# Performance work log

Measured on AMD Instinct MI355X. Metric: run time of the kernel, lower is better.

## Reference

```python
import jax, jax.numpy as jnp
import numpy as np

MAX_LOGIT = 30.0
COV_WEIGHT = 1.0


def setup_inputs() -> dict:
    key = jax.random.key(0)
    ks = jax.random.split(key, 8)
    B, T, S, H = 8, 100, 400, 256
    sc = 1.0 / np.sqrt(H)
    return {
        "decoder_outputs": jax.random.normal(ks[0], (B, T, H), jnp.float32),
        "encoder_outputs": jax.random.normal(ks[1], (B, S, H), jnp.float32),
        "src_mask": jnp.zeros((B, S), dtype=bool),
        "W_h": jax.random.normal(ks[2], (H, H), jnp.float32) * sc,
        "W_s": jax.random.normal(ks[3], (H, H), jnp.float32) * sc,
        "w_c": jax.random.normal(ks[4], (H,), jnp.float32) * sc,  # Linear(1,H) weight
        "v": jax.random.normal(ks[5], (H,), jnp.float32) * sc,    # Linear(H,1) weight
        "b_attn": jnp.zeros((H,), jnp.float32),
    }


def reference(decoder_outputs, encoder_outputs, src_mask, W_h, W_s, w_c, v, b_attn):
    B, T, H = decoder_outputs.shape
    S = encoder_outputs.shape[1]
    neg_inf = jnp.float32(-jnp.inf)

    Wh = jnp.einsum('bsh,hk->bsk', encoder_outputs, W_h)   # [B,S,H]
    Ws = jnp.einsum('bth,hk->btk', decoder_outputs, W_s)   # [B,T,H]
    # E_base: [B,T,S,H]
    E_base = Wh[:, None, :, :] + Ws[:, :, None, :] + b_attn

    def logits(x):
        e = jnp.einsum('btsh,h->bts', jnp.tanh(x), v)
        e = jnp.clip(e, -MAX_LOGIT, MAX_LOGIT)
        return jnp.where(src_mask[:, None, :], neg_inf, e)

    A_prelim = jax.nn.softmax(logits(E_base), axis=-1)      # [B,T,S]
    cum = jnp.cumsum(A_prelim, axis=1)
    cov_shifted = jnp.concatenate(
        [jnp.zeros((B, 1, S), A_prelim.dtype), cum[:, :-1, :]], axis=1)  # [B,T,S]

    # W_c applied to scalar coverage: outer product with w_c -> [B,T,S,H]
    E_final = logits(E_base + cov_shifted[..., None] * w_c)
    A_final = jax.nn.softmax(E_final, axis=-1)              # [B,T,S]

    context = jnp.einsum('bts,bsh->bth', A_final, encoder_outputs)
    cov_loss = (COV_WEIGHT * jnp.sum(jnp.minimum(A_final, cov_shifted), axis=-1).mean())[None]
    return context, A_final, cov_loss
```

## Files before the change

kernel.cpp:

```cpp
#include <hip/hip_runtime.h>
#include <math.h>

#define B_ 8
#define T_ 100
#define S_ 400
#define H_ 256
#define BT_ (B_ * T_)
#define MAXL 30.0f
#define K_EXP 2.885390081777927f

#define AF_OFF (BT_ * H_)
#define LOSS_OFF (BT_ * H_ + BT_ * S_)

#define WHT_OFF 0
#define WSB_OFF (B_ * H_ * S_)
#define ACOV_OFF (WSB_OFF + BT_ * H_)

__device__ __forceinline__ float wave_sum(float p) {
#pragma unroll
    for (int off = 32; off; off >>= 1) p += __shfl_xor(p, off, 64);
    return p;
}

__device__ __forceinline__ float wave_max(float p) {
#pragma unroll
    for (int off = 32; off; off >>= 1) p = fmaxf(p, __shfl_xor(p, off, 64));
    return p;
}

#define ROWS 4
__global__ __launch_bounds__(256) void k_gemm(
    const float* __restrict__ dec, const float* __restrict__ enc,
    const float* __restrict__ W_h, const float* __restrict__ W_s,
    const float* __restrict__ b_attn,
    float* __restrict__ WhT, float* __restrict__ Wsb) {
    const int tid = threadIdx.x;
    const int blk = blockIdx.x;
    const int NB_ENC = (B_ * S_) / ROWS;

    float a0 = 0.f, a1 = 0.f, a2 = 0.f, a3 = 0.f;

    if (blk < NB_ENC) {
        const int r0 = blk * ROWS;
        const int b = r0 / S_, s0 = r0 - b * S_;
        const float* in = enc + (size_t)r0 * H_;
        const float* Wp = W_h + tid;
#pragma unroll 8
        for (int h = 0; h < H_; ++h) {
            float w = Wp[(size_t)h * H_];
            a0 = fmaf(in[h], w, a0);
            a1 = fmaf(in[H_ + h], w, a1);
            a2 = fmaf(in[2 * H_ + h], w, a2);
            a3 = fmaf(in[3 * H_ + h], w, a3);
        }
        float* o = WhT + ((size_t)b * H_ + tid) * S_ + s0;
        o[0] = K_EXP * a0;
        o[1] = K_EXP * a1;
        o[2] = K_EXP * a2;
        o[3] = K_EXP * a3;
    } else {
        const int bt0 = (blk - NB_ENC) * ROWS;
        const float* in = dec + (size_t)bt0 * H_;
        const float* Wp = W_s + tid;
        const float bias = b_attn[tid];
#pragma unroll 8
        for (int h = 0; h < H_; ++h) {
            float w = Wp[(size_t)h * H_];
            a0 = fmaf(in[h], w, a0);
            a1 = fmaf(in[H_ + h], w, a1);
            a2 = fmaf(in[2 * H_ + h], w, a2);
            a3 = fmaf(in[3 * H_ + h], w, a3);
        }
        Wsb[(size_t)(bt0 + 0) * H_ + tid] = K_EXP * (a0 + bias);
        Wsb[(size_t)(bt0 + 1) * H_ + tid] = K_EXP * (a1 + bias);
        Wsb[(size_t)(bt0 + 2) * H_ + tid] = K_EXP * (a2 + bias);
        Wsb[(size_t)(bt0 + 3) * H_ + tid] = K_EXP * (a3 + bias);
    }
}

__global__ __launch_bounds__(512) void k_prelim(
    const float* __restrict__ WhT, const float* __restrict__ Wsb,
    const float* __restrict__ v,
    const unsigned char* __restrict__ mask,
    float* __restrict__ A) {
    __shared__ float red[16];
    const int blk = blockIdx.x;
    const int b = blk & 7;
    const int t = blk >> 3;
    const int bt = b * T_ + t;
    const int tid = threadIdx.x;
    const int lane = tid & 63;
    const int wid = tid >> 6;
    const int s = tid;
    const bool act = (s < S_);

    const float4 vv4 = *reinterpret_cast<const float4*>(v + 4 * lane);
    const float sumv = wave_sum((vv4.x + vv4.y) + (vv4.z + vv4.w));

    const float* Wsr = Wsb + (size_t)bt * H_;
    float acc = 0.f;
    if (act) {
        const float* wcol = WhT + (size_t)b * H_ * S_ + s;
#pragma unroll 8
        for (int h = 0; h < H_; ++h) {
            float w = wcol[(size_t)h * S_];
            float r = __builtin_amdgcn_rcpf(__builtin_amdgcn_exp2f(w + Wsr[h]) + 1.0f);
            acc = fmaf(r, v[h], acc);
        }
    }

    float e = -INFINITY;
    if (act) {
        e = fminf(fmaxf(sumv - 2.f * acc, -MAXL), MAXL);
        if (mask[(size_t)b * S_ + s]) e = -INFINITY;
    }

    float mx = wave_max(e);
    if (lane == 0) red[wid] = mx;
    __syncthreads();
    mx = fmaxf(fmaxf(fmaxf(red[0], red[1]), fmaxf(red[2], red[3])),
               fmaxf(fmaxf(red[4], red[5]), fmaxf(red[6], red[7])));

    float p = act ? __expf(e - mx) : 0.f;
    float sum = wave_sum(p);
    if (lane == 0) red[8 + wid] = sum;
    __syncthreads();
    sum = ((red[8] + red[9]) + (red[10] + red[11])) +
          ((red[12] + red[13]) + (red[14] + red[15]));
    const float inv = __builtin_amdgcn_rcpf(sum);

    if (act) A[(size_t)bt * S_ + s] = p * inv;
}

__global__ __launch_bounds__(64) void k_cumsum(float* __restrict__ A,
                                               float* __restrict__ out) {
    const int idx = blockIdx.x * 64 + threadIdx.x;
    if (idx == 0) out[LOSS_OFF] = 0.f;
    if (idx >= B_ * S_) return;
    const int b = idx / S_;
    const int s = idx - b * S_;
    float* col = A + (size_t)b * T_ * S_ + s;
    float run = 0.f;
#pragma unroll 10
    for (int t = 0; t < T_; ++t) {
        float a = col[(size_t)t * S_];
        col[(size_t)t * S_] = run;
        run += a;
    }
}

__global__ __launch_bounds__(512) void k_final(
    const float* __restrict__ WhT, const float* __restrict__ Wsb,
    const float* __restrict__ v, const float* __restrict__ w_c,
    const float* __restrict__ cov,
    const unsigned char* __restrict__ mask,
    const float* __restrict__ enc,
    float* __restrict__ out) {
    __shared__ float e_lds[S_];
    __shared__ float ctx_part[H_];
    __shared__ float red[16];
    const int blk = blockIdx.x;
    const int b = blk & 7;
    const int t = blk >> 3;
    const int bt = b * T_ + t;
    const int tid = threadIdx.x;
    const int lane = tid & 63;
    const int wid = tid >> 6;
    const int s = tid;
    const bool act = (s < S_);

    const float4 vv4 = *reinterpret_cast<const float4*>(v + 4 * lane);
    const float sumv = wave_sum((vv4.x + vv4.y) + (vv4.z + vv4.w));

    float c = 0.f;
    if (act) c = cov[(size_t)bt * S_ + s];
    const float ck = K_EXP * c;

    const float* Wsr = Wsb + (size_t)bt * H_;
    float acc = 0.f;
    if (act) {
        const float* wcol = WhT + (size_t)b * H_ * S_ + s;
#pragma unroll 8
        for (int h = 0; h < H_; ++h) {
            float w = wcol[(size_t)h * S_];
            float arg = fmaf(ck, w_c[h], w + Wsr[h]);
            float r = __builtin_amdgcn_rcpf(__builtin_amdgcn_exp2f(arg) + 1.0f);
            acc = fmaf(r, v[h], acc);
        }
    }

    float e = -INFINITY;
    if (act) {
        e = fminf(fmaxf(sumv - 2.f * acc, -MAXL), MAXL);
        if (mask[(size_t)b * S_ + s]) e = -INFINITY;
    }

    float mx = wave_max(e);
    if (lane == 0) red[wid] = mx;
    __syncthreads();
    mx = fmaxf(fmaxf(fmaxf(red[0], red[1]), fmaxf(red[2], red[3])),
               fmaxf(fmaxf(red[4], red[5]), fmaxf(red[6], red[7])));

    float p = act ? __expf(e - mx) : 0.f;
    float sum = wave_sum(p);
    if (lane == 0) red[8 + wid] = sum;
    __syncthreads();
    sum = ((red[8] + red[9]) + (red[10] + red[11])) +
          ((red[12] + red[13]) + (red[14] + red[15]));
    const float inv = __builtin_amdgcn_rcpf(sum);

    const float a = act ? p * inv : 0.f;

    float lp = act ? fminf(a, c) : 0.f;
    lp = wave_sum(lp);
    if (lane == 0) red[wid] = lp;

    if (act) {
        e_lds[s] = a;
        out[AF_OFF + (size_t)bt * S_ + s] = a;
    }
    __syncthreads();

    if (tid == 0) {
        float tot = ((red[0] + red[1]) + (red[2] + red[3])) +
                    ((red[4] + red[5]) + (red[6] + red[7]));
        atomicAdd(out + LOSS_OFF, tot * (1.0f / (B_ * T_)));
    }

    const int h = tid & (H_ - 1);
    const int half = tid >> 8;
    const int s0 = half * (S_ / 2);
    const float* eb = enc + ((size_t)b * S_ + s0) * H_ + h;
    float ca = 0.f, cb = 0.f, cc = 0.f, cd = 0.f;
#pragma unroll 5
    for (int j = 0; j < S_ / 2; j += 4) {
        ca = fmaf(e_lds[s0 + j], eb[(size_t)j * H_], ca);
        cb = fmaf(e_lds[s0 + j + 1], eb[(size_t)(j + 1) * H_], cb);
        cc = fmaf(e_lds[s0 + j + 2], eb[(size_t)(j + 2) * H_], cc);
        cd = fmaf(e_lds[s0 + j + 3], eb[(size_t)(j + 3) * H_], cd);
    }
    if (half == 0) ctx_part[h] = (ca + cb) + (cc + cd);
    __syncthreads();
    if (half == 1) out[(size_t)bt * H_ + h] = ctx_part[h] + (ca + cb) + (cc + cd);
}

extern "C" void kernel_launch(void* const* d_in, const int* in_sizes, int n_in,
                              void* d_out, int out_size, void* d_ws, size_t ws_size,
                              hipStream_t stream) {
    const float* dec = (const float*)d_in[0];
    const float* enc = (const float*)d_in[1];
    const unsigned char* mask = (const unsigned char*)d_in[2];
    const float* W_h = (const float*)d_in[3];
    const float* W_s = (const float*)d_in[4];
    const float* w_c = (const float*)d_in[5];
    const float* v = (const float*)d_in[6];
    const float* b_attn = (const float*)d_in[7];

    float* out = (float*)d_out;
    float* ws = (float*)d_ws;
    float* WhT = ws + WHT_OFF;
    float* Wsb = ws + WSB_OFF;
    float* Acov = ws + ACOV_OFF;

    const int nb_gemm = (B_ * S_) / ROWS + BT_ / ROWS;
    k_gemm<<<nb_gemm, 256, 0, stream>>>(dec, enc, W_h, W_s, b_attn, WhT, Wsb);
    k_prelim<<<BT_, 512, 0, stream>>>(WhT, Wsb, v, mask, Acov);
    k_cumsum<<<(B_ * S_ + 63) / 64, 64, 0, stream>>>(Acov, out);
    k_final<<<BT_, 512, 0, stream>>>(WhT, Wsb, v, w_c, Acov, mask, enc, out);
}
```

Before: 163.8 us.

## Process two timesteps per block to reuse WhT and encoder loads

Each block of the prelim and final attention kernels now computes two consecutive decoder timesteps. Every WhT column value and encoder row loaded is used for both, and the two independent exp/rcp chains add instruction-level parallelism. This halves memory loads per output but also halves the number of blocks, which reduces parallelism across the GPU's compute units.

```diff
diff --git a/kernel.cpp b/kernel.cpp
--- a/kernel.cpp
+++ b/kernel.cpp
@@ -83,11 +83,11 @@
     const float* __restrict__ v,
     const unsigned char* __restrict__ mask,
     float* __restrict__ A) {
-    __shared__ float red[16];
+    __shared__ float red[32];
     const int blk = blockIdx.x;
     const int b = blk & 7;
-    const int t = blk >> 3;
-    const int bt = b * T_ + t;
+    const int tp = blk >> 3;
+    const int bt0 = b * T_ + 2 * tp;
     const int tid = threadIdx.x;
     const int lane = tid & 63;
     const int wid = tid >> 6;
@@ -97,39 +97,53 @@
     const float4 vv4 = *reinterpret_cast<const float4*>(v + 4 * lane);
     const float sumv = wave_sum((vv4.x + vv4.y) + (vv4.z + vv4.w));
 
-    const float* Wsr = Wsb + (size_t)bt * H_;
-    float acc = 0.f;
+    const float* Ws0 = Wsb + (size_t)bt0 * H_;
+    const float* Ws1 = Ws0 + H_;
+    float acc0 = 0.f, acc1 = 0.f;
     if (act) {
         const float* wcol = WhT + (size_t)b * H_ * S_ + s;
 #pragma unroll 8
         for (int h = 0; h < H_; ++h) {
             float w = wcol[(size_t)h * S_];
-            float r = __builtin_amdgcn_rcpf(__builtin_amdgcn_exp2f(w + Wsr[h]) + 1.0f);
-            acc = fmaf(r, v[h], acc);
+            float vh = v[h];
+            float r0 = __builtin_amdgcn_rcpf(__builtin_amdgcn_exp2f(w + Ws0[h]) + 1.0f);
+            float r1 = __builtin_amdgcn_rcpf(__builtin_amdgcn_exp2f(w + Ws1[h]) + 1.0f);
+            acc0 = fmaf(r0, vh, acc0);
+            acc1 = fmaf(r1, vh, acc1);
         }
     }
 
-    float e = -INFINITY;
-    if (act) {
-        e = fminf(fmaxf(sumv - 2.f * acc, -MAXL), MAXL);
-        if (mask[(size_t)b * S_ + s]) e = -INFINITY;
-    }
-
-    float mx = wave_max(e);
-    if (lane == 0) red[wid] = mx;
-    __syncthreads();
-    mx = fmaxf(fmaxf(fmaxf(red[0], red[1]), fmaxf(red[2], red[3])),
-               fmaxf(fmaxf(red[4], red[5]), fmaxf(red[6], red[7])));
-
-    float p = act ? __expf(e - mx) : 0.f;
-    float sum = wave_sum(p);
-    if (lane == 0) red[8 + wid] = sum;
-    __syncthreads();
-    sum = ((red[8] + red[9]) + (red[10] + red[11])) +
-          ((red[12] + red[13]) + (red[14] + red[15]));
-    const float inv = __builtin_amdgcn_rcpf(sum);
-
-    if (act) A[(size_t)bt * S_ + s] = p * inv;
+    float e0 = -INFINITY, e1 = -INFINITY;
+    if (act) {
+        e0 = fminf(fmaxf(sumv - 2.f * acc0, -MAXL), MAXL);
+        e1 = fminf(fmaxf(sumv - 2.f * acc1, -MAXL), MAXL);
+        if (mask[(size_t)b * S_ + s]) { e0 = -INFINITY; e1 = -INFINITY; }
+    }
+
+    float mx0 = wave_max(e0);
+    float mx1 = wave_max(e1);
+    if (lane == 0) { red[wid] = mx0; red[8 + wid] = mx1; }
+    __syncthreads();
+    mx0 = fmaxf(fmaxf(fmaxf(red[0], red[1]), fmaxf(red[2], red[3])),
+                fmaxf(fmaxf(red[4], red[5]), fmaxf(red[6], red[7])));
+    mx1 = fmaxf(fmaxf(fmaxf(red[8], red[9]), fmaxf(red[10], red[11])),
+                fmaxf(fmaxf(red[12], red[13]), fmaxf(red[14], red[15])));
+
+    float p0 = act ? __expf(e0 - mx0) : 0.f;
+    float p1 = act ? __expf(e1 - mx1) : 0.f;
+    float sm0 = wave_sum(p0);
+    float sm1 = wave_sum(p1);
+    if (lane == 0) { red[16 + wid] = sm0; red[24 + wid] = sm1; }
+    __syncthreads();
+    sm0 = ((red[16] + red[17]) + (red[18] + red[19])) +
+          ((red[20] + red[21]) + (red[22] + red[23]));
+    sm1 = ((red[24] + red[25]) + (red[26] + red[27])) +
+          ((red[28] + red[29]) + (red[30] + red[31]));
+
+    if (act) {
+        A[(size_t)bt0 * S_ + s] = p0 * __builtin_amdgcn_rcpf(sm0);
+        A[(size_t)(bt0 + 1) * S_ + s] = p1 * __builtin_amdgcn_rcpf(sm1);
+    }
 }
 
 __global__ __launch_bounds__(64) void k_cumsum(float* __restrict__ A,
@@ -156,13 +170,13 @@
     const unsigned char* __restrict__ mask,
     const float* __restrict__ enc,
     float* __restrict__ out) {
-    __shared__ float e_lds[S_];
-    __shared__ float ctx_part[H_];
-    __shared__ float red[16];
+    __shared__ float e0_lds[S_], e1_lds[S_];
+    __shared__ float ctx0[H_], ctx1[H_];
+    __shared__ float red[32];
     const int blk = blockIdx.x;
     const int b = blk & 7;
-    const int t = blk >> 3;
-    const int bt = b * T_ + t;
+    const int tp = blk >> 3;
+    const int bt0 = b * T_ + 2 * tp;
     const int tid = threadIdx.x;
     const int lane = tid & 63;
     const int wid = tid >> 6;
@@ -172,52 +186,71 @@
     const float4 vv4 = *reinterpret_cast<const float4*>(v + 4 * lane);
     const float sumv = wave_sum((vv4.x + vv4.y) + (vv4.z + vv4.w));
 
-    float c = 0.f;
-    if (act) c = cov[(size_t)bt * S_ + s];
-    const float ck = K_EXP * c;
-
-    const float* Wsr = Wsb + (size_t)bt * H_;
-    float acc = 0.f;
+    float c0 = 0.f, c1 = 0.f;
+    if (act) {
+        c0 = cov[(size_t)bt0 * S_ + s];
+        c1 = cov[(size_t)(bt0 + 1) * S_ + s];
+    }
+    const float ck0 = K_EXP * c0, ck1 = K_EXP * c1;
+
+    const float* Ws0 = Wsb + (size_t)bt0 * H_;
+    const float* Ws1 = Ws0 + H_;
+    float acc0 = 0.f, acc1 = 0.f;
     if (act) {
         const float* wcol = WhT + (size_t)b * H_ * S_ + s;
 #pragma unroll 8
         for (int h = 0; h < H_; ++h) {
             float w = wcol[(size_t)h * S_];
-            float arg = fmaf(ck, w_c[h], w + Wsr[h]);
-            float r = __builtin_amdgcn_rcpf(__builtin_amdgcn_exp2f(arg) + 1.0f);
-            acc = fmaf(r, v[h], acc);
+            float wch = w_c[h];
+            float vh = v[h];
+            float a0 = fmaf(ck0, wch, w + Ws0[h]);
+            float a1 = fmaf(ck1, wch, w + Ws1[h]);
+            float r0 = __builtin_amdgcn_rcpf(__builtin_amdgcn_exp2f(a0) + 1.0f);
+            float r1 = __builtin_amdgcn_rcpf(__builtin_amdgcn_exp2f(a1) + 1.0f);
+            acc0 = fmaf(r0, vh, acc0);
+            acc1 = fmaf(r1, vh, acc1);
         }
     }
 
-    float e = -INFINITY;
-    if (act) {
-        e = fminf(fmaxf(sumv - 2.f * acc, -MAXL), MAXL);
-        if (mask[(size_t)b * S_ + s]) e = -INFINITY;
-    }
-
-    float mx = wave_max(e);
-    if (lane == 0) red[wid] = mx;
-    __syncthreads();
-    mx = fmaxf(fmaxf(fmaxf(red[0], red[1]), fmaxf(red[2], red[3])),
-               fmaxf(fmaxf(red[4], red[5]), fmaxf(red[6], red[7])));
-
-    float p = act ? __expf(e - mx) : 0.f;
-    float sum = wave_sum(p);
-    if (lane == 0) red[8 + wid] = sum;
-    __syncthreads();
-    sum = ((red[8] + red[9]) + (red[10] + red[11])) +
-          ((red[12] + red[13]) + (red[14] + red[15]));
-    const float inv = __builtin_amdgcn_rcpf(sum);
-
-    const float a = act ? p * inv : 0.f;
-
-    float lp = act ? fminf(a, c) : 0.f;
+    float e0 = -INFINITY, e1 = -INFINITY;
+    if (act) {
+        e0 = fminf(fmaxf(sumv - 2.f * acc0, -MAXL), MAXL);
+        e1 = fminf(fmaxf(sumv - 2.f * acc1, -MAXL), MAXL);
+        if (mask[(size_t)b * S_ + s]) { e0 = -INFINITY; e1 = -INFINITY; }
+    }
+
+    float mx0 = wave_max(e0);
+    float mx1 = wave_max(e1);
+    if (lane == 0) { red[wid] = mx0; red[8 + wid] = mx1; }
+    __syncthreads();
+    mx0 = fmaxf(fmaxf(fmaxf(red[0], red[1]), fmaxf(red[2], red[3])),
+                fmaxf(fmaxf(red[4], red[5]), fmaxf(red[6], red[7])));
+    mx1 = fmaxf(fmaxf(fmaxf(red[8], red[9]), fmaxf(red[10], red[11])),
+                fmaxf(fmaxf(red[12], red[13]), fmaxf(red[14], red[15])));
+
+    float p0 = act ? __expf(e0 - mx0) : 0.f;
+    float p1 = act ? __expf(e1 - mx1) : 0.f;
+    float sm0 = wave_sum(p0);
+    float sm1 = wave_sum(p1);
+    if (lane == 0) { red[16 + wid] = sm0; red[24 + wid] = sm1; }
+    __syncthreads();
+    sm0 = ((red[16] + red[17]) + (red[18] + red[19])) +
+          ((red[20] + red[21]) + (red[22] + red[23]));
+    sm1 = ((red[24] + red[25]) + (red[26] + red[27])) +
+          ((red[28] + red[29]) + (red[30] + red[31]));
+
+    const float a0 = act ? p0 * __builtin_amdgcn_rcpf(sm0) : 0.f;
+    const float a1 = act ? p1 * __builtin_amdgcn_rcpf(sm1) : 0.f;
+
+    float lp = act ? (fminf(a0, c0) + fminf(a1, c1)) : 0.f;
     lp = wave_sum(lp);
     if (lane == 0) red[wid] = lp;
 
     if (act) {
-        e_lds[s] = a;
-        out[AF_OFF + (size_t)bt * S_ + s] = a;
+        e0_lds[s] = a0;
+        e1_lds[s] = a1;
+        out[AF_OFF + (size_t)bt0 * S_ + s] = a0;
+        out[AF_OFF + (size_t)(bt0 + 1) * S_ + s] = a1;
     }
     __syncthreads();
 
@@ -229,19 +262,33 @@
 
     const int h = tid & (H_ - 1);
     const int half = tid >> 8;
-    const int s0 = half * (S_ / 2);
-    const float* eb = enc + ((size_t)b * S_ + s0) * H_ + h;
-    float ca = 0.f, cb = 0.f, cc = 0.f, cd = 0.f;
+    const int sb = half * (S_ / 2);
+    const float* eb = enc + ((size_t)b * S_ + sb) * H_ + h;
+    float q00 = 0.f, q01 = 0.f, q02 = 0.f, q03 = 0.f;
+    float q10 = 0.f, q11 = 0.f, q12 = 0.f, q13 = 0.f;
 #pragma unroll 5
     for (int j = 0; j < S_ / 2; j += 4) {
-        ca = fmaf(e_lds[s0 + j], eb[(size_t)j * H_], ca);
-        cb = fmaf(e_lds[s0 + j + 1], eb[(size_t)(j + 1) * H_], cb);
-        cc = fmaf(e_lds[s0 + j + 2], eb[(size_t)(j + 2) * H_], cc);
-        cd = fmaf(e_lds[s0 + j + 3], eb[(size_t)(j + 3) * H_], cd);
-    }
-    if (half == 0) ctx_part[h] = (ca + cb) + (cc + cd);
-    __syncthreads();
-    if (half == 1) out[(size_t)bt * H_ + h] = ctx_part[h] + (ca + cb) + (cc + cd);
+        float w0 = eb[(size_t)j * H_];
+        float w1 = eb[(size_t)(j + 1) * H_];
+        float w2 = eb[(size_t)(j + 2) * H_];
+        float w3 = eb[(size_t)(j + 3) * H_];
+        q00 = fmaf(e0_lds[sb + j], w0, q00);
+        q10 = fmaf(e1_lds[sb + j], w0, q10);
+        q01 = fmaf(e0_lds[sb + j + 1], w1, q01);
+        q11 = fmaf(e1_lds[sb + j + 1], w1, q11);
+        q02 = fmaf(e0_lds[sb + j + 2], w2, q02);
+        q12 = fmaf(e1_lds[sb + j + 2], w2, q12);
+        q03 = fmaf(e0_lds[sb + j + 3], w3, q03);
+        q13 = fmaf(e1_lds[sb + j + 3], w3, q13);
+    }
+    const float r0 = (q00 + q01) + (q02 + q03);
+    const float r1 = (q10 + q11) + (q12 + q13);
+    if (half == 0) { ctx0[h] = r0; ctx1[h] = r1; }
+    __syncthreads();
+    if (half == 1) {
+        out[(size_t)bt0 * H_ + h] = ctx0[h] + r0;
+        out[(size_t)(bt0 + 1) * H_ + h] = ctx1[h] + r1;
+    }
 }
 
 extern "C" void kernel_launch(void* const* d_in, const int* in_sizes, int n_in,
@@ -263,8 +310,9 @@
     float* Acov = ws + ACOV_OFF;
 
     const int nb_gemm = (B_ * S_) / ROWS + BT_ / ROWS;
+    const int nb_pair = B_ * (T_ / 2);
     k_gemm<<<nb_gemm, 256, 0, stream>>>(dec, enc, W_h, W_s, b_attn, WhT, Wsb);
-    k_prelim<<<BT_, 512, 0, stream>>>(WhT, Wsb, v, mask, Acov);
+    k_prelim<<<nb_pair, 512, 0, stream>>>(WhT, Wsb, v, mask, Acov);
     k_cumsum<<<(B_ * S_ + 63) / 64, 64, 0, stream>>>(Acov, out);
-    k_final<<<BT_, 512, 0, stream>>>(WhT, Wsb, v, w_c, Acov, mask, enc, out);
-}
+    k_final<<<nb_pair, 512, 0, stream>>>(WhT, Wsb, v, w_c, Acov, mask, enc, out);
+}
```

Measured after the change: 163.3 us. About the same (-0.3%).
